# Kernel optimization log

Hardware: AMD Instinct MI355X
Metric: run time of the kernel (lower is better)

The kernel has to match this reference:

```python
import jax, jax.numpy as jnp
import numpy as np

N_NODES = 100000
N_EDGES = 3200000
IN_DIM, HID, N_LAB = 128, 64, 121


def setup_inputs() -> dict:
    key = jax.random.key(0)
    ks = jax.random.split(key, 8)
    x = jax.random.normal(ks[0], (N_NODES, IN_DIM), dtype=jnp.float32)
    edge_index = jax.random.randint(ks[1], (2, N_EDGES), 0, N_NODES, dtype=jnp.int64)
    W1 = jax.random.normal(ks[2], (IN_DIM, HID), dtype=jnp.float32) * (1.0 / np.sqrt(IN_DIM))
    b1 = jnp.zeros((HID,), dtype=jnp.float32)
    W2 = jax.random.normal(ks[3], (HID, HID), dtype=jnp.float32) * (1.0 / np.sqrt(HID))
    b2 = jnp.zeros((HID,), dtype=jnp.float32)
    Wout = jax.random.normal(ks[4], (HID, N_LAB), dtype=jnp.float32) * (1.0 / np.sqrt(HID))
    bout = jnp.zeros((N_LAB,), dtype=jnp.float32)
    return {"x": x, "edge_index": edge_index, "W1": W1, "b1": b1,
            "W2": W2, "b2": b2, "Wout": Wout, "bout": bout}


def _gcn_conv(x, W, b, src, dst, norm, n):
    # x' = D^{-1/2}(A+I)D^{-1/2} X W + b  (edges already include self-loops)
    xw = x @ W                                   # [N, out]
    msg = xw[src] * norm[:, None]                # [E+N, out] gather + scale
    agg = jax.ops.segment_sum(msg, dst, num_segments=n)  # scatter-add
    return agg + b


def reference(x, edge_index, W1, b1, W2, b2, Wout, bout):
    n = x.shape[0]
    loop = jnp.arange(n, dtype=edge_index.dtype)
    src = jnp.concatenate([edge_index[0], loop])
    dst = jnp.concatenate([edge_index[1], loop])
    # symmetric normalization (self-loops guarantee deg >= 1)
    deg = jax.ops.segment_sum(jnp.ones_like(dst, dtype=x.dtype), dst, num_segments=n)
    dinv = jax.lax.rsqrt(deg)
    norm = dinv[src] * dinv[dst]                 # [E+N]

    h = jax.nn.relu(_gcn_conv(x, W1, b1, src, dst, norm, n))
    # dropout p=0.5 is identity in eval mode (training=False)
    h = jax.nn.relu(_gcn_conv(h, W2, b2, src, dst, norm, n))
    logits = h @ Wout + bout                     # [N, num_labels]
    return logits
```

## Files before the change

kernel.cpp:

```cpp
#include <hip/hip_runtime.h>
#include <hip/hip_bf16.h>
#include <hip/hip_fp16.h>


#define IN_DIM 128
#define HID 64
#define N_LAB 121
#define NB_BLK 256

__global__ void scan1(const int* __restrict__ in, int* __restrict__ out,
                      int* __restrict__ bsums, int n) {
    __shared__ int s[256];
    int i = blockIdx.x * 256 + threadIdx.x;
    int v = (i < n) ? in[i] : 0;
    s[threadIdx.x] = v;
    __syncthreads();
    for (int off = 1; off < 256; off <<= 1) {
        int t = (threadIdx.x >= off) ? s[threadIdx.x - off] : 0;
        __syncthreads();
        s[threadIdx.x] += t;
        __syncthreads();
    }
    if (i < n) out[i] = s[threadIdx.x] - v;
    if (threadIdx.x == 255) bsums[blockIdx.x] = s[255];
}

__global__ void scan2(int* __restrict__ bsums, int nb) {
    __shared__ int s[512];
    int v = (threadIdx.x < nb) ? bsums[threadIdx.x] : 0;
    s[threadIdx.x] = v;
    __syncthreads();
    for (int off = 1; off < 512; off <<= 1) {
        int t = (threadIdx.x >= off) ? s[threadIdx.x - off] : 0;
        __syncthreads();
        s[threadIdx.x] += t;
        __syncthreads();
    }
    if (threadIdx.x < nb) bsums[threadIdx.x] = s[threadIdx.x] - v;
}

__global__ void scan_add(int* __restrict__ out, const int* __restrict__ bsums, int n) {
    int i = blockIdx.x * 256 + threadIdx.x;
    if (i < n) out[i] += bsums[blockIdx.x];
}

__global__ __launch_bounds__(256) void bucket_count(const int* __restrict__ dst,
                                                    int* __restrict__ counts,
                                                    int nbuk, int chunk, int E) {
    extern __shared__ int c[];
    for (int j = threadIdx.x; j < nbuk; j += 256) c[j] = 0;
    __syncthreads();
    int beg = blockIdx.x * chunk;
    int end = min(beg + chunk, E);
    for (int i = beg + threadIdx.x; i < end; i += 256)
        atomicAdd(&c[dst[i] >> 8], 1);
    __syncthreads();
    for (int j = threadIdx.x; j < nbuk; j += 256)
        counts[j * NB_BLK + blockIdx.x] = c[j];
}

__global__ __launch_bounds__(256) void bucket_scatter(const int* __restrict__ src,
                                                      const int* __restrict__ dst,
                                                      const int* __restrict__ base,
                                                      int* __restrict__ bucketed,
                                                      int nbuk, int chunk, int E) {
    extern __shared__ int c[];
    for (int j = threadIdx.x; j < nbuk; j += 256) c[j] = 0;
    __syncthreads();
    int beg = blockIdx.x * chunk;
    int end = min(beg + chunk, E);
    for (int i = beg + threadIdx.x; i < end; i += 256) {
        int d = dst[i];
        int b = d >> 8;
        int r = atomicAdd(&c[b], 1);
        int pos = base[b * NB_BLK + blockIdx.x] + r;
        bucketed[pos] = ((d & 255) << 17) | src[i];
    }
}

__global__ __launch_bounds__(256) void bucket_sort(const int* __restrict__ bucketed,
                                                   const int* __restrict__ base,
                                                   int* __restrict__ srcs,
                                                   int* __restrict__ row_ptr,
                                                   float* __restrict__ dinv,
                                                   int nbuk, int N, int E) {
    __shared__ int h[256];
    __shared__ int cur[256];
    int b = blockIdx.x;
    int nodeBase = b << 8;
    int s = base[b * NB_BLK];
    int e = (b == nbuk - 1) ? E : base[(b + 1) * NB_BLK];
    h[threadIdx.x] = 0;
    __syncthreads();
    for (int i = s + threadIdx.x; i < e; i += 256)
        atomicAdd(&h[bucketed[i] >> 17], 1);
    __syncthreads();
    int v = h[threadIdx.x];
    for (int off = 1; off < 256; off <<= 1) {
        int t = (threadIdx.x >= off) ? h[threadIdx.x - off] : 0;
        __syncthreads();
        h[threadIdx.x] += t;
        __syncthreads();
    }
    int excl = h[threadIdx.x] - v;
    cur[threadIdx.x] = excl;
    int node = nodeBase + threadIdx.x;
    if (node < N) {
        row_ptr[node] = s + excl;
        dinv[node] = rsqrtf((float)v + 1.0f);
    }
    if (b == nbuk - 1 && threadIdx.x == 0) row_ptr[N] = E;
    __syncthreads();
    for (int i = s + threadIdx.x; i < e; i += 256) {
        int p = bucketed[i];
        int d = p >> 17;
        int r = atomicAdd(&cur[d], 1);
        srcs[s + r] = p & 0x1FFFF;
    }
}

template <int K, int N, typename OT>
__global__ __launch_bounds__(256) void gemm_kernel(
        const float* __restrict__ A, const float* __restrict__ B,
        const float* __restrict__ bias, const float* __restrict__ rowscale,
        OT* __restrict__ C, int M) {
    constexpr int ROWS = 64;
    constexpr int NPAD = (N <= 64) ? 64 : 128;
    constexpr int CG = NPAD / 4;
    constexpr int RG = 256 / CG;
    constexpr int RPT = ROWS / RG;
    __shared__ float Bs[K * NPAD];
    __shared__ float As[ROWS * K];

    for (int i = threadIdx.x; i < K * NPAD; i += 256) {
        int c = i & (NPAD - 1);
        int k = i / NPAD;
        Bs[i] = (c < N) ? B[k * N + c] : 0.f;
    }
    const int row_base = blockIdx.x * ROWS;
    const float* Ablk = A + (size_t)row_base * K;
    int avail = (M - row_base) * K;
    if (avail > ROWS * K) avail = ROWS * K;
    const int nvec = avail >> 2;
    const float4* __restrict__ Av = (const float4*)Ablk;
    float4* Asv = (float4*)As;
    for (int i = threadIdx.x; i < nvec; i += 256) Asv[i] = Av[i];
    __syncthreads();

    const int cg = threadIdx.x % CG;
    const int rg = threadIdx.x / CG;

    float acc[RPT][4];
    #pragma unroll
    for (int j = 0; j < RPT; ++j) {
        acc[j][0] = 0.f; acc[j][1] = 0.f; acc[j][2] = 0.f; acc[j][3] = 0.f;
    }

    for (int k = 0; k < K; k += 4) {
        float4 Bq[4];
        #pragma unroll
        for (int kk = 0; kk < 4; ++kk)
            Bq[kk] = *(const float4*)&Bs[(k + kk) * NPAD + cg * 4];
        #pragma unroll
        for (int j = 0; j < RPT; ++j) {
            const float4 Aq = *(const float4*)&As[(rg + RG * j) * K + k];
            #pragma unroll
            for (int c = 0; c < 4; ++c) {
                const float b0 = ((const float*)&Bq[0])[c];
                const float b1 = ((const float*)&Bq[1])[c];
                const float b2 = ((const float*)&Bq[2])[c];
                const float b3 = ((const float*)&Bq[3])[c];
                float a = acc[j][c];
                a = fmaf(Aq.x, b0, a);
                a = fmaf(Aq.y, b1, a);
                a = fmaf(Aq.z, b2, a);
                a = fmaf(Aq.w, b3, a);
                acc[j][c] = a;
            }
        }
    }

    float bv[4];
    #pragma unroll
    for (int c = 0; c < 4; ++c) {
        int col = cg * 4 + c;
        bv[c] = (bias && col < N) ? bias[col] : 0.f;
    }

    #pragma unroll
    for (int j = 0; j < RPT; ++j) {
        const int r = row_base + rg + RG * j;
        if (r >= M) continue;
        const float sc = rowscale ? rowscale[r] : 1.0f;
        float o[4];
        #pragma unroll
        for (int c = 0; c < 4; ++c) o[c] = fmaf(acc[j][c], sc, bv[c]);
        OT* Crow = C + (size_t)r * N;
        if constexpr (sizeof(OT) == 4 && (N % 4 == 0)) {
            *(float4*)&Crow[cg * 4] = make_float4(o[0], o[1], o[2], o[3]);
        } else if constexpr (sizeof(OT) == 2 && (N % 4 == 0)) {
            __half2* p = (__half2*)&Crow[cg * 4];
            p[0] = __floats2half2_rn(o[0], o[1]);
            p[1] = __floats2half2_rn(o[2], o[3]);
        } else {
            #pragma unroll
            for (int c = 0; c < 4; ++c) {
                int col = cg * 4 + c;
                if (col < N) Crow[col] = (OT)o[c];
            }
        }
    }
}

__global__ __launch_bounds__(256) void aggregate(
        const __half* __restrict__ feat2, const int* __restrict__ rp,
        const int* __restrict__ srcs, const float* __restrict__ dinv,
        const float* __restrict__ bias, float* __restrict__ out, int N) {
    const int wid = (int)((((size_t)blockIdx.x * 256) + threadIdx.x) >> 6);
    if (wid >= N) return;
    const int lane = threadIdx.x & 63;
    const int slot = lane >> 3;
    const int oct  = lane & 7;
    const size_t fbase = (size_t)oct << 3;

    float acc[8];
    #pragma unroll
    for (int i = 0; i < 8; ++i) acc[i] = 0.f;

    if (slot == 0) {
        const uint4 raw = *(const uint4*)(feat2 + (((size_t)wid << 6) + fbase));
        const __half2* h = (const __half2*)&raw;
        #pragma unroll
        for (int i = 0; i < 4; ++i) {
            const float2 f = __half22float2(h[i]);
            acc[2 * i]     += f.x;
            acc[2 * i + 1] += f.y;
        }
    }

    const int beg = rp[wid], end = rp[wid + 1];
    int e = beg;
    for (; e + 16 <= end; e += 16) {
        const int s0 = srcs[e + slot];
        const int s1 = srcs[e + 8 + slot];
        const uint4 r0 = *(const uint4*)(feat2 + (((size_t)s0 << 6) + fbase));
        const uint4 r1 = *(const uint4*)(feat2 + (((size_t)s1 << 6) + fbase));
        const __half2* h0 = (const __half2*)&r0;
        const __half2* h1 = (const __half2*)&r1;
        #pragma unroll
        for (int i = 0; i < 4; ++i) {
            const float2 f0 = __half22float2(h0[i]);
            const float2 f1 = __half22float2(h1[i]);
            acc[2 * i]     += f0.x + f1.x;
            acc[2 * i + 1] += f0.y + f1.y;
        }
    }
    for (; e < end; e += 8) {
        const int idx = e + slot;
        if (idx < end) {
            const int s = srcs[idx];
            const uint4 r0 = *(const uint4*)(feat2 + (((size_t)s << 6) + fbase));
            const __half2* h0 = (const __half2*)&r0;
            #pragma unroll
            for (int i = 0; i < 4; ++i) {
                const float2 f = __half22float2(h0[i]);
                acc[2 * i]     += f.x;
                acc[2 * i + 1] += f.y;
            }
        }
    }

    #pragma unroll
    for (int m = 8; m <= 32; m <<= 1) {
        #pragma unroll
        for (int i = 0; i < 8; ++i)
            acc[i] += __shfl_xor(acc[i], m, 64);
    }

    if (slot == 0) {
        const float sc = dinv[wid];
        float o[8];
        #pragma unroll
        for (int i = 0; i < 8; ++i)
            o[i] = fmaxf(fmaf(acc[i], sc, bias[fbase + i]), 0.f);
        float4* dst4 = (float4*)(out + (((size_t)wid << 6) + fbase));
        dst4[0] = make_float4(o[0], o[1], o[2], o[3]);
        dst4[1] = make_float4(o[4], o[5], o[6], o[7]);
    }
}

extern "C" void kernel_launch(void* const* d_in, const int* in_sizes, int n_in,
                              void* d_out, int out_size, void* d_ws, size_t ws_size,
                              hipStream_t stream) {
    const float* x    = (const float*)d_in[0];
    const int*   ei   = (const int*)d_in[1];
    const float* W1   = (const float*)d_in[2];
    const float* b1   = (const float*)d_in[3];
    const float* W2   = (const float*)d_in[4];
    const float* b2   = (const float*)d_in[5];
    const float* Wout = (const float*)d_in[6];
    const float* bout = (const float*)d_in[7];
    float* out = (float*)d_out;

    const int N = in_sizes[0] / IN_DIM;
    const int E = in_sizes[1] / 2;
    const int* srcI = ei;
    const int* dstI = ei + E;

    const int nbuk = (N + 255) >> 8;
    const int M1 = nbuk * NB_BLK;
    const int chunk = (E + NB_BLK - 1) / NB_BLK;

    int*    row_ptr = (int*)d_ws;
    float*  dinv    = (float*)(row_ptr + (N + 1));
    int*    counts  = (int*)(dinv + N);
    int*    base    = counts + M1;
    int*    bsums2  = base + M1;
    int*    srcs    = bsums2 + 512;
    __half* feat2   = (__half*)(((uintptr_t)(srcs + E) + 15) & ~(uintptr_t)15);
    float*  hbuf    = (float*)(feat2 + (size_t)N * HID);
    int*    bucketed = (int*)feat2;

    const int nbM = (M1 + 255) / 256;
    const int gemmBlocks = (N + 63) / 64;
    const int aggBlocks = (int)(((size_t)N * HID + 255) / 256);
    const size_t ldsBuk = (size_t)nbuk * sizeof(int);

    bucket_count<<<NB_BLK, 256, ldsBuk, stream>>>(dstI, counts, nbuk, chunk, E);
    scan1<<<nbM, 256, 0, stream>>>(counts, base, bsums2, M1);
    scan2<<<1, 512, 0, stream>>>(bsums2, nbM);
    scan_add<<<nbM, 256, 0, stream>>>(base, bsums2, M1);
    bucket_scatter<<<NB_BLK, 256, ldsBuk, stream>>>(srcI, dstI, base, bucketed, nbuk, chunk, E);
    bucket_sort<<<nbuk, 256, 0, stream>>>(bucketed, base, srcs, row_ptr, dinv, nbuk, N, E);

    gemm_kernel<IN_DIM, HID, __half><<<gemmBlocks, 256, 0, stream>>>(x, W1, nullptr, dinv, feat2, N);
    aggregate<<<aggBlocks, 256, 0, stream>>>(feat2, row_ptr, srcs, dinv, b1, hbuf, N);

    gemm_kernel<HID, HID, __half><<<gemmBlocks, 256, 0, stream>>>(hbuf, W2, nullptr, dinv, feat2, N);
    aggregate<<<aggBlocks, 256, 0, stream>>>(feat2, row_ptr, srcs, dinv, b2, hbuf, N);

    gemm_kernel<HID, N_LAB, float><<<gemmBlocks, 256, 0, stream>>>(hbuf, Wout, bout, nullptr, out, N);
}
```

Measured before the change: 522.7 us.

## Double bucketing blocks, pre-shift source offsets, read GEMM A directly, predicate aggregate loop

```diff
diff --git a/kernel.cpp b/kernel.cpp
--- a/kernel.cpp
+++ b/kernel.cpp
@@ -6,7 +6,7 @@
 #define IN_DIM 128
 #define HID 64
 #define N_LAB 121
-#define NB_BLK 256
+#define NB_BLK 512
 
 __global__ void scan1(const int* __restrict__ in, int* __restrict__ out,
                       int* __restrict__ bsums, int n) {
@@ -25,18 +25,18 @@
     if (threadIdx.x == 255) bsums[blockIdx.x] = s[255];
 }
 
-__global__ void scan2(int* __restrict__ bsums, int nb) {
-    __shared__ int s[512];
-    int v = (threadIdx.x < nb) ? bsums[threadIdx.x] : 0;
+__global__ __launch_bounds__(1024) void scan2(int* __restrict__ bsums, int nb) {
+    __shared__ int s[1024];
+    int v = (threadIdx.x < (unsigned)nb) ? bsums[threadIdx.x] : 0;
     s[threadIdx.x] = v;
     __syncthreads();
-    for (int off = 1; off < 512; off <<= 1) {
+    for (int off = 1; off < 1024; off <<= 1) {
         int t = (threadIdx.x >= off) ? s[threadIdx.x - off] : 0;
         __syncthreads();
         s[threadIdx.x] += t;
         __syncthreads();
     }
-    if (threadIdx.x < nb) bsums[threadIdx.x] = s[threadIdx.x] - v;
+    if (threadIdx.x < (unsigned)nb) bsums[threadIdx.x] = s[threadIdx.x] - v;
 }
 
 __global__ void scan_add(int* __restrict__ out, const int* __restrict__ bsums, int n) {
@@ -115,7 +115,7 @@
         int p = bucketed[i];
         int d = p >> 17;
         int r = atomicAdd(&cur[d], 1);
-        srcs[s + r] = p & 0x1FFFF;
+        srcs[s + r] = (p & 0x1FFFF) << 7;
     }
 }
 
@@ -130,25 +130,25 @@
     constexpr int RG = 256 / CG;
     constexpr int RPT = ROWS / RG;
     __shared__ float Bs[K * NPAD];
-    __shared__ float As[ROWS * K];
 
     for (int i = threadIdx.x; i < K * NPAD; i += 256) {
         int c = i & (NPAD - 1);
         int k = i / NPAD;
         Bs[i] = (c < N) ? B[k * N + c] : 0.f;
     }
-    const int row_base = blockIdx.x * ROWS;
-    const float* Ablk = A + (size_t)row_base * K;
-    int avail = (M - row_base) * K;
-    if (avail > ROWS * K) avail = ROWS * K;
-    const int nvec = avail >> 2;
-    const float4* __restrict__ Av = (const float4*)Ablk;
-    float4* Asv = (float4*)As;
-    for (int i = threadIdx.x; i < nvec; i += 256) Asv[i] = Av[i];
     __syncthreads();
 
     const int cg = threadIdx.x % CG;
     const int rg = threadIdx.x / CG;
+    const int row_base = blockIdx.x * ROWS;
+
+    const float* Arow[RPT];
+    #pragma unroll
+    for (int j = 0; j < RPT; ++j) {
+        int r = row_base + rg + RG * j;
+        if (r > M - 1) r = M - 1;
+        Arow[j] = A + (size_t)r * K;
+    }
 
     float acc[RPT][4];
     #pragma unroll
@@ -163,7 +163,7 @@
             Bq[kk] = *(const float4*)&Bs[(k + kk) * NPAD + cg * 4];
         #pragma unroll
         for (int j = 0; j < RPT; ++j) {
-            const float4 Aq = *(const float4*)&As[(rg + RG * j) * K + k];
+            const float4 Aq = *(const float4*)(Arow[j] + k);
             #pragma unroll
             for (int c = 0; c < 4; ++c) {
                 const float b0 = ((const float*)&Bq[0])[c];
@@ -221,15 +221,15 @@
     const int lane = threadIdx.x & 63;
     const int slot = lane >> 3;
     const int oct  = lane & 7;
-    const size_t fbase = (size_t)oct << 3;
+    const char* fbB = (const char*)feat2 + oct * 16;
 
     float acc[8];
     #pragma unroll
     for (int i = 0; i < 8; ++i) acc[i] = 0.f;
 
     if (slot == 0) {
-        const uint4 raw = *(const uint4*)(feat2 + (((size_t)wid << 6) + fbase));
-        const __half2* h = (const __half2*)&raw;
+        const uint4 q = *(const uint4*)(fbB + ((size_t)wid << 7));
+        const __half2* h = (const __half2*)&q;
         #pragma unroll
         for (int i = 0; i < 4; ++i) {
             const float2 f = __half22float2(h[i]);
@@ -239,14 +239,20 @@
     }
 
     const int beg = rp[wid], end = rp[wid + 1];
-    int e = beg;
-    for (; e + 16 <= end; e += 16) {
-        const int s0 = srcs[e + slot];
-        const int s1 = srcs[e + 8 + slot];
-        const uint4 r0 = *(const uint4*)(feat2 + (((size_t)s0 << 6) + fbase));
-        const uint4 r1 = *(const uint4*)(feat2 + (((size_t)s1 << 6) + fbase));
-        const __half2* h0 = (const __half2*)&r0;
-        const __half2* h1 = (const __half2*)&r1;
+    int idx = beg + slot;
+    while (__any(idx < end)) {
+        const bool p0 = idx < end;
+        const bool p1 = (idx + 8) < end;
+        const int i0 = p0 ? idx : beg;
+        const int i1 = p1 ? (idx + 8) : beg;
+        const int o0 = srcs[i0];
+        const int o1 = srcs[i1];
+        uint4 q0 = *(const uint4*)(fbB + o0);
+        uint4 q1 = *(const uint4*)(fbB + o1);
+        if (!p0) { q0.x = 0u; q0.y = 0u; q0.z = 0u; q0.w = 0u; }
+        if (!p1) { q1.x = 0u; q1.y = 0u; q1.z = 0u; q1.w = 0u; }
+        const __half2* h0 = (const __half2*)&q0;
+        const __half2* h1 = (const __half2*)&q1;
         #pragma unroll
         for (int i = 0; i < 4; ++i) {
             const float2 f0 = __half22float2(h0[i]);
@@ -254,20 +260,7 @@
             acc[2 * i]     += f0.x + f1.x;
             acc[2 * i + 1] += f0.y + f1.y;
         }
-    }
-    for (; e < end; e += 8) {
-        const int idx = e + slot;
-        if (idx < end) {
-            const int s = srcs[idx];
-            const uint4 r0 = *(const uint4*)(feat2 + (((size_t)s << 6) + fbase));
-            const __half2* h0 = (const __half2*)&r0;
-            #pragma unroll
-            for (int i = 0; i < 4; ++i) {
-                const float2 f = __half22float2(h0[i]);
-                acc[2 * i]     += f.x;
-                acc[2 * i + 1] += f.y;
-            }
-        }
+        idx += 16;
     }
 
     #pragma unroll
@@ -282,10 +275,10 @@
         float o[8];
         #pragma unroll
         for (int i = 0; i < 8; ++i)
-            o[i] = fmaxf(fmaf(acc[i], sc, bias[fbase + i]), 0.f);
-        float4* dst4 = (float4*)(out + (((size_t)wid << 6) + fbase));
-        dst4[0] = make_float4(o[0], o[1], o[2], o[3]);
-        dst4[1] = make_float4(o[4], o[5], o[6], o[7]);
+            o[i] = fmaxf(fmaf(acc[i], sc, bias[oct * 8 + i]), 0.f);
+        float4* d4 = (float4*)(out + (((size_t)wid << 6) + oct * 8));
+        d4[0] = make_float4(o[0], o[1], o[2], o[3]);
+        d4[1] = make_float4(o[4], o[5], o[6], o[7]);
     }
 }
 
@@ -316,7 +309,7 @@
     int*    counts  = (int*)(dinv + N);
     int*    base    = counts + M1;
     int*    bsums2  = base + M1;
-    int*    srcs    = bsums2 + 512;
+    int*    srcs    = bsums2 + 1024;
     __half* feat2   = (__half*)(((uintptr_t)(srcs + E) + 15) & ~(uintptr_t)15);
     float*  hbuf    = (float*)(feat2 + (size_t)N * HID);
     int*    bucketed = (int*)feat2;
@@ -328,7 +321,7 @@
 
     bucket_count<<<NB_BLK, 256, ldsBuk, stream>>>(dstI, counts, nbuk, chunk, E);
     scan1<<<nbM, 256, 0, stream>>>(counts, base, bsums2, M1);
-    scan2<<<1, 512, 0, stream>>>(bsums2, nbM);
+    scan2<<<1, 1024, 0, stream>>>(bsums2, nbM);
     scan_add<<<nbM, 256, 0, stream>>>(base, bsums2, M1);
     bucket_scatter<<<NB_BLK, 256, ldsBuk, stream>>>(srcI, dstI, base, bucketed, nbuk, chunk, E);
     bucket_sort<<<nbuk, 256, 0, stream>>>(bucketed, base, srcs, row_ptr, dinv, nbuk, N, E);
```

New measurement: 511.3 us. 2.2% less time.
